# Performance work log

Hardware: AMD Instinct MI355X
Metric: run time of the kernel (lower is better)

## Reference

```python
import jax, jax.numpy as jnp
import numpy as np

D_MODEL = 1024
HEADS = 16
D_K = D_MODEL // HEADS
B, S = 2, 2048


def setup_inputs() -> dict:
    key = jax.random.key(0)
    ks = jax.random.split(key, 11)
    sc = 1.0 / np.sqrt(D_MODEL)
    return {
        "q": jax.random.normal(ks[0], (B, S, D_MODEL), jnp.float32),
        "k": jax.random.normal(ks[1], (B, S, D_MODEL), jnp.float32),
        "v": jax.random.normal(ks[2], (B, S, D_MODEL), jnp.float32),
        "Wq": jax.random.normal(ks[3], (D_MODEL, D_MODEL), jnp.float32) * sc,
        "bq": jnp.zeros((D_MODEL,), jnp.float32),
        "Wk": jax.random.normal(ks[4], (D_MODEL, D_MODEL), jnp.float32) * sc,
        "bk": jnp.zeros((D_MODEL,), jnp.float32),
        "Wv": jax.random.normal(ks[5], (D_MODEL, D_MODEL), jnp.float32) * sc,
        "bv": jnp.zeros((D_MODEL,), jnp.float32),
        "Wo": jax.random.normal(ks[6], (D_MODEL, D_MODEL), jnp.float32) * sc,
        "bo": jnp.zeros((D_MODEL,), jnp.float32),
    }


def reference(q, k, v, Wq, bq, Wk, bk, Wv, bv, Wo, bo):
    bs = q.shape[0]
    # linear projections then split heads: [B,S,D] -> [B,H,S,Dk]
    def proj(x, W, b):
        y = x @ W.T + b
        return y.reshape(bs, -1, HEADS, D_K).transpose(0, 2, 1, 3)

    qh = proj(q, Wq, bq)
    kh = proj(k, Wk, bk)
    vh = proj(v, Wv, bv)
    # scores: [B,H,Sq,Sk] -- full attention matrix as in the original
    scores = jnp.einsum("bhqd,bhkd->bhqk", qh, kh) / jnp.sqrt(
        jnp.asarray(D_K, jnp.float32))
    attn = jax.nn.softmax(scores, axis=-1)
    # dropout is identity in eval/reference mode
    out = jnp.einsum("bhqk,bhkd->bhqd", attn, vh)
    concat = out.transpose(0, 2, 1, 3).reshape(bs, -1, D_MODEL)
    return concat @ Wo.T + bo
```

## Files before the change

### kernel.cpp

```cpp
#include <hip/hip_runtime.h>
#include <hip/hip_bf16.h>

typedef __attribute__((ext_vector_type(8))) short bf16x8;
typedef __attribute__((ext_vector_type(4))) float f32x4;

#define DM   1024
#define SEQ  2048
#define NB   2
#define NH   16
#define MR   (NB*SEQ)

#define SMK  (MR*DM)
#define W1M  (DM*DM)

#define QSCALE 0.18033688011112042f

#define OFF_QB  ((size_t)0)
#define OFF_KB  ((size_t)SMK)
#define OFF_VB  ((size_t)(2*(size_t)SMK))
#define OFF_WQ  ((size_t)(3*(size_t)SMK))
#define OFF_WO  ((size_t)(3*(size_t)SMK + 3*(size_t)W1M))
#define OFF_QP  ((size_t)(3*(size_t)SMK + 4*(size_t)W1M))
#define OFF_KP  ((size_t)(4*(size_t)SMK + 4*(size_t)W1M))
#define OFF_VP  ((size_t)(5*(size_t)SMK + 4*(size_t)W1M))
#define OFF_CC  ((size_t)0)

__device__ __forceinline__ unsigned short f2bf(float f) {
  union { __hip_bfloat16 b; unsigned short u; } cv;
  cv.b = __float2bfloat16(f);
  return cv.u;
}

__global__ __launch_bounds__(256) void cvt_inputs(const float* __restrict__ q,
                                                  const float* __restrict__ k,
                                                  const float* __restrict__ v,
                                                  unsigned short* __restrict__ dst) {
  const int z = blockIdx.y;
  const float* src = (z == 0) ? q : ((z == 1) ? k : v);
  int i = blockIdx.x * 256 + threadIdx.x;
  float4 val = reinterpret_cast<const float4*>(src)[i];
  ushort4 o;
  o.x = f2bf(val.x); o.y = f2bf(val.y); o.z = f2bf(val.z); o.w = f2bf(val.w);
  reinterpret_cast<ushort4*>(dst + (size_t)z * SMK)[i] = o;
}

__global__ __launch_bounds__(256) void cvt_weights(const float* __restrict__ wq,
                                                   const float* __restrict__ wk,
                                                   const float* __restrict__ wv,
                                                   const float* __restrict__ wo,
                                                   unsigned short* __restrict__ dst) {
  const int z = blockIdx.y;
  const float* src = (z == 0) ? wq : ((z == 1) ? wk : ((z == 2) ? wv : wo));
  int i = blockIdx.x * 256 + threadIdx.x;
  float4 val = reinterpret_cast<const float4*>(src)[i];
  ushort4 o;
  o.x = f2bf(val.x); o.y = f2bf(val.y); o.z = f2bf(val.z); o.w = f2bf(val.w);
  reinterpret_cast<ushort4*>(dst + (size_t)z * W1M)[i] = o;
}

__device__ __forceinline__ void gload_lds16(const void* g, void* l) {
  __builtin_amdgcn_global_load_lds(
      (const __attribute__((address_space(1))) unsigned int*)g,
      (__attribute__((address_space(3))) unsigned int*)l,
      16, 0, 0);
}

template<int BM, int BN, bool OUT_BF16, bool BIAS_ROW>
__device__ __forceinline__ void gemm_bt_body(unsigned short* __restrict__ As,
                                             unsigned short* __restrict__ Bs,
                                             const unsigned short* __restrict__ A,
                                             const unsigned short* __restrict__ Bt,
                                             const float* __restrict__ bias,
                                             void* __restrict__ Cv,
                                             int N, int K, float scale,
                                             int brow, int bcol) {
  constexpr int MREP = BM / 32;
  constexpr int NREP = BN / 32;
  const int tid  = threadIdx.x;
  const int lane = tid & 63;
  const int w    = tid >> 6;
  const int wr   = w >> 1, wc = w & 1;

  f32x4 acc[MREP][NREP];
#pragma unroll
  for (int m = 0; m < MREP; m++)
#pragma unroll
    for (int n = 0; n < NREP; n++) acc[m][n] = (f32x4){0.f, 0.f, 0.f, 0.f};

  const int srow = lane >> 2;
  const int scol = (lane & 3) * 8;

  auto stage = [&](int buf, int k0) {
#pragma unroll
    for (int c = w; c < BM / 16; c += 4)
      gload_lds16(A + (size_t)(brow + c * 16 + srow) * K + k0 + scol,
                  (char*)As + (size_t)buf * BM * 64 + c * 1024);
#pragma unroll
    for (int c = w; c < BN / 16; c += 4)
      gload_lds16(Bt + (size_t)(bcol + c * 16 + srow) * K + k0 + scol,
                  (char*)Bs + (size_t)buf * BN * 64 + c * 1024);
  };

  stage(0, 0);
  __syncthreads();

  const int nk = K / 32;
  const int lrow_a = wr * (BM / 2) + (lane & 15);
  const int lrow_b = wc * (BN / 2) + (lane & 15);
  const int lcol   = (lane >> 4) * 8;

  for (int kt = 0; kt < nk; ++kt) {
    int buf = kt & 1;
    if (kt + 1 < nk) stage(buf ^ 1, (kt + 1) * 32);
    bf16x8 a[MREP], b[NREP];
#pragma unroll
    for (int m = 0; m < MREP; m++)
      a[m] = *(const bf16x8*)&As[(size_t)buf * BM * 32 + (lrow_a + m * 16) * 32 + lcol];
#pragma unroll
    for (int n = 0; n < NREP; n++)
      b[n] = *(const bf16x8*)&Bs[(size_t)buf * BN * 32 + (lrow_b + n * 16) * 32 + lcol];
    __builtin_amdgcn_s_setprio(1);
#pragma unroll
    for (int m = 0; m < MREP; m++)
#pragma unroll
      for (int n = 0; n < NREP; n++)
        acc[m][n] = __builtin_amdgcn_mfma_f32_16x16x32_bf16(a[m], b[n], acc[m][n], 0, 0, 0);
    __builtin_amdgcn_s_setprio(0);
    __syncthreads();
  }

  const int crow0 = brow + wr * (BM / 2);
  const int ccol0 = bcol + wc * (BN / 2);
  const int rsub  = (lane >> 4) * 4;
  const int csub  = lane & 15;
#pragma unroll
  for (int m = 0; m < MREP; m++)
#pragma unroll
    for (int n = 0; n < NREP; n++) {
      int col = ccol0 + n * 16 + csub;
      float bcol_v = BIAS_ROW ? 0.f : bias[col];
#pragma unroll
      for (int q = 0; q < 4; q++) {
        int row = crow0 + m * 16 + rsub + q;
        float bb = BIAS_ROW ? bias[row] : bcol_v;
        float v = (acc[m][n][q] + bb) * scale;
        if (OUT_BF16)
          ((unsigned short*)Cv)[(size_t)row * N + col] = f2bf(v);
        else
          ((float*)Cv)[(size_t)row * N + col] = v;
      }
    }
}

__global__ __launch_bounds__(256) void gemm_qkv(unsigned short* ws,
                                                const float* __restrict__ bq,
                                                const float* __restrict__ bk,
                                                const float* __restrict__ bv) {
  __shared__ unsigned short As[2 * 128 * 32];
  __shared__ unsigned short Bs[2 * 128 * 32];
  const int z = blockIdx.z;
  const int bid = blockIdx.x;
  if (z < 2) {
    int bx = bid & 7, by = bid >> 3;
    gemm_bt_body<128, 128, true, false>(
        As, Bs,
        ws + OFF_QB + (size_t)z * SMK, ws + OFF_WQ + (size_t)z * W1M,
        z ? bk : bq, ws + OFF_QP + (size_t)z * SMK,
        DM, DM, z ? 1.f : QSCALE, by * 128, bx * 128);
  } else {
    int bx = bid & 31, by = bid >> 5;
    gemm_bt_body<128, 128, true, true>(
        As, Bs,
        ws + OFF_WQ + 2 * W1M, ws + OFF_VB,
        bv, ws + OFF_VP,
        MR, DM, 1.f, by * 128, bx * 128);
  }
}

__global__ __launch_bounds__(256) void gemm_out(const unsigned short* __restrict__ ws,
                                                const float* __restrict__ bo,
                                                float* __restrict__ out) {
  __shared__ unsigned short As[2 * 64 * 32];
  __shared__ unsigned short Bs[2 * 128 * 32];
  gemm_bt_body<64, 128, false, false>(
      As, Bs,
      ws + OFF_CC, ws + OFF_WO, bo, out,
      DM, DM, 1.f, blockIdx.y * 64, blockIdx.x * 128);
}

__global__ __launch_bounds__(256) void flash_attn(unsigned short* ws) {
  __shared__ unsigned short Ks[2][64 * 64];
  __shared__ unsigned short Vs[2][64 * 64];
  __shared__ unsigned short Ps[4][32 * 64];

  const int tid  = threadIdx.x;
  const int lane = tid & 63;
  const int w    = tid >> 6;
  const int g    = lane >> 4;
  const int ql   = lane & 15;
  const int bid  = blockIdx.x;
  const int swzb = (bid & 7) * 64 + (bid >> 3);
  const int qblk = swzb & 15;
  const int bh   = swzb >> 4;
  const int b    = bh >> 4, h = bh & 15;

  const unsigned short* Qp = ws + OFF_QP;
  const unsigned short* Kp = ws + OFF_KP;
  const unsigned short* Vp = ws + OFF_VP;
  unsigned short* CC = ws + OFF_CC;

  const unsigned short* Kg = Kp + (size_t)(b * SEQ) * DM + h * 64;
  const unsigned short* Vg = Vp + (size_t)(h * 64) * MR + (size_t)b * SEQ;

  bf16x8 aq[2][2];
#pragma unroll
  for (int s = 0; s < 2; s++) {
    const unsigned short* qrow =
        Qp + (size_t)(b * SEQ + qblk * 128 + w * 32 + s * 16 + ql) * DM + h * 64;
    aq[s][0] = *(const bf16x8*)(qrow + g * 8);
    aq[s][1] = *(const bf16x8*)(qrow + 32 + g * 8);
  }

  const bf16x8 kOnes = {16256, 16256, 16256, 16256, 16256, 16256, 16256, 16256};

  f32x4 o_acc[2][4];
  f32x4 o_l[2];
#pragma unroll
  for (int s = 0; s < 2; s++) {
    o_l[s] = (f32x4){0.f, 0.f, 0.f, 0.f};
#pragma unroll
    for (int d = 0; d < 4; d++) o_acc[s][d] = (f32x4){0.f, 0.f, 0.f, 0.f};
  }

  auto stage = [&](unsigned short* lds, const unsigned short* gbase, int stride) {
#pragma unroll
    for (int sh = 0; sh < 2; sh++) {
      int slot = sh * 256 + w * 64 + lane;
      int srow = slot >> 3;
      int gch  = (slot & 7) ^ (srow & 7);
      gload_lds16(gbase + (size_t)srow * stride + gch * 8,
                  (char*)lds + (size_t)(sh * 256 + w * 64) * 16);
    }
  };

  stage(Ks[0], Kg, DM);
  stage(Vs[0], Vg, MR);

  unsigned short* Pw = &Ps[w][0];
  const int swq = ql & 7;

  for (int kt = 0; kt < SEQ / 64; ++kt) {
    int buf = kt & 1;
    __syncthreads();
    if (kt + 1 < SEQ / 64) {
      stage(Ks[buf ^ 1], Kg + (size_t)(kt + 1) * 64 * DM, DM);
      stage(Vs[buf ^ 1], Vg + (kt + 1) * 64, MR);
    }
    const unsigned short* Kb = Ks[buf];
    const unsigned short* Vb = Vs[buf];

    f32x4 st[2][4];
#pragma unroll
    for (int s = 0; s < 2; s++)
#pragma unroll
      for (int f = 0; f < 4; f++) st[s][f] = (f32x4){0.f, 0.f, 0.f, 0.f};
    __builtin_amdgcn_s_setprio(1);
#pragma unroll
    for (int kk = 0; kk < 2; kk++)
#pragma unroll
      for (int f = 0; f < 4; f++) {
        int sr = f * 16 + ql;
        bf16x8 ak = *(const bf16x8*)&Kb[sr * 64 + (((kk * 4 + g) ^ swq) << 3)];
        st[0][f] = __builtin_amdgcn_mfma_f32_16x16x32_bf16(ak, aq[0][kk], st[0][f], 0, 0, 0);
        st[1][f] = __builtin_amdgcn_mfma_f32_16x16x32_bf16(ak, aq[1][kk], st[1][f], 0, 0, 0);
      }
    __builtin_amdgcn_s_setprio(0);

#pragma unroll
    for (int s = 0; s < 2; s++)
#pragma unroll
      for (int f = 0; f < 4; f++) {
        ushort4 pv;
        pv.x = f2bf(__builtin_amdgcn_exp2f(st[s][f][0]));
        pv.y = f2bf(__builtin_amdgcn_exp2f(st[s][f][1]));
        pv.z = f2bf(__builtin_amdgcn_exp2f(st[s][f][2]));
        pv.w = f2bf(__builtin_amdgcn_exp2f(st[s][f][3]));
        int chunk = (f << 1) + (g >> 1);
        Pw[0] = Pw[0];
        *(ushort4*)&Pw[(s * 16 + ql) * 64 + ((chunk ^ swq) << 3) + ((g & 1) << 2)] = pv;
      }

#pragma unroll
    for (int kk = 0; kk < 2; kk++) {
      bf16x8 pb0 = *(const bf16x8*)&Pw[ql * 64 + (((kk * 4 + g) ^ swq) << 3)];
      bf16x8 pb1 = *(const bf16x8*)&Pw[(16 + ql) * 64 + (((kk * 4 + g) ^ swq) << 3)];
      __builtin_amdgcn_s_setprio(1);
      o_l[0] = __builtin_amdgcn_mfma_f32_16x16x32_bf16(kOnes, pb0, o_l[0], 0, 0, 0);
      o_l[1] = __builtin_amdgcn_mfma_f32_16x16x32_bf16(kOnes, pb1, o_l[1], 0, 0, 0);
#pragma unroll
      for (int db = 0; db < 4; db++) {
        int dr = db * 16 + ql;
        bf16x8 va = *(const bf16x8*)&Vb[dr * 64 + (((kk * 4 + g) ^ swq) << 3)];
        o_acc[0][db] = __builtin_amdgcn_mfma_f32_16x16x32_bf16(va, pb0, o_acc[0][db], 0, 0, 0);
        o_acc[1][db] = __builtin_amdgcn_mfma_f32_16x16x32_bf16(va, pb1, o_acc[1][db], 0, 0, 0);
      }
      __builtin_amdgcn_s_setprio(0);
    }
  }

#pragma unroll
  for (int s = 0; s < 2; s++) {
    float inv = 1.f / o_l[s][0];
    int qg = b * SEQ + qblk * 128 + w * 32 + s * 16 + ql;
    unsigned short* crow = CC + (size_t)qg * DM + h * 64;
#pragma unroll
    for (int db = 0; db < 4; db++) {
      ushort4 o;
      o.x = f2bf(o_acc[s][db][0] * inv);
      o.y = f2bf(o_acc[s][db][1] * inv);
      o.z = f2bf(o_acc[s][db][2] * inv);
      o.w = f2bf(o_acc[s][db][3] * inv);
      *(ushort4*)&crow[db * 16 + g * 4] = o;
    }
  }
}

extern "C" void kernel_launch(void* const* d_in, const int* in_sizes, int n_in,
                              void* d_out, int out_size, void* d_ws, size_t ws_size,
                              hipStream_t stream) {
  const float* q  = (const float*)d_in[0];
  const float* k  = (const float*)d_in[1];
  const float* v  = (const float*)d_in[2];
  const float* Wq = (const float*)d_in[3];
  const float* bq = (const float*)d_in[4];
  const float* Wk = (const float*)d_in[5];
  const float* bk = (const float*)d_in[6];
  const float* Wv = (const float*)d_in[7];
  const float* bv = (const float*)d_in[8];
  const float* Wo = (const float*)d_in[9];
  const float* bo = (const float*)d_in[10];

  unsigned short* ws = (unsigned short*)d_ws;
  float* out = (float*)d_out;

  cvt_inputs<<<dim3(SMK / 1024, 3), dim3(256), 0, stream>>>(q, k, v, ws + OFF_QB);
  cvt_weights<<<dim3(W1M / 1024, 4), dim3(256), 0, stream>>>(Wq, Wk, Wv, Wo, ws + OFF_WQ);

  gemm_qkv<<<dim3(256, 1, 3), dim3(256), 0, stream>>>(ws, bq, bk, bv);

  flash_attn<<<dim3(512), dim3(256), 0, stream>>>(ws);

  gemm_out<<<dim3(DM / 128, MR / 64, 1), dim3(256), 0, stream>>>(ws, bo, out);
}
```

Before: 128.3 us.

## Use 32x32x16 MFMA in flash attention and keep P in registers via permlane swap

The attention inner loop moves from 16x16x32 to 32x32x16 bf16 MFMA tiles, with each wave handling 32 query rows as a single tile. The probability tile is packed to bf16 with v_cvt_pk_bf16_f32 and rearranged across lane halves with v_permlane32_swap, so it is no longer written to and read back from LDS. The row sum is now accumulated with scalar adds instead of an extra MFMA against a ones vector. This is meant to remove the LDS round trip and the extra MFMAs, at the cost of more accumulator registers and exact lane-layout assumptions that must match the MFMA operand format.

New measurement: 132.7 us. 3.4% more time.

```diff
diff --git a/kernel.cpp b/kernel.cpp
--- a/kernel.cpp
+++ b/kernel.cpp
@@ -3,6 +3,7 @@
 
 typedef __attribute__((ext_vector_type(8))) short bf16x8;
 typedef __attribute__((ext_vector_type(4))) float f32x4;
+typedef __attribute__((ext_vector_type(16))) float f32x16;
 
 #define DM   1024
 #define SEQ  2048
@@ -29,6 +30,16 @@
   union { __hip_bfloat16 b; unsigned short u; } cv;
   cv.b = __float2bfloat16(f);
   return cv.u;
+}
+
+__device__ __forceinline__ unsigned int cvtpk_bf16(float lo, float hi) {
+  unsigned int r;
+  asm("v_cvt_pk_bf16_f32 %0, %1, %2" : "=v"(r) : "v"(lo), "v"(hi));
+  return r;
+}
+
+__device__ __forceinline__ void plane32_swap(unsigned int& a, unsigned int& b) {
+  asm("v_permlane32_swap_b32 %0, %1" : "+v"(a), "+v"(b));
 }
 
 __global__ __launch_bounds__(256) void cvt_inputs(const float* __restrict__ q,
@@ -191,13 +202,13 @@
 __global__ __launch_bounds__(256) void flash_attn(unsigned short* ws) {
   __shared__ unsigned short Ks[2][64 * 64];
   __shared__ unsigned short Vs[2][64 * 64];
-  __shared__ unsigned short Ps[4][32 * 64];
 
   const int tid  = threadIdx.x;
   const int lane = tid & 63;
   const int w    = tid >> 6;
-  const int g    = lane >> 4;
-  const int ql   = lane & 15;
+  const int q    = lane & 31;
+  const int hi   = lane >> 5;
+  const int swq  = q & 7;
   const int bid  = blockIdx.x;
   const int swzb = (bid & 7) * 64 + (bid >> 3);
   const int qblk = swzb & 15;
@@ -212,25 +223,21 @@
   const unsigned short* Kg = Kp + (size_t)(b * SEQ) * DM + h * 64;
   const unsigned short* Vg = Vp + (size_t)(h * 64) * MR + (size_t)b * SEQ;
 
-  bf16x8 aq[2][2];
-#pragma unroll
-  for (int s = 0; s < 2; s++) {
+  bf16x8 bqf[4];
+  {
     const unsigned short* qrow =
-        Qp + (size_t)(b * SEQ + qblk * 128 + w * 32 + s * 16 + ql) * DM + h * 64;
-    aq[s][0] = *(const bf16x8*)(qrow + g * 8);
-    aq[s][1] = *(const bf16x8*)(qrow + 32 + g * 8);
+        Qp + (size_t)(b * SEQ + qblk * 128 + w * 32 + q) * DM + h * 64;
+#pragma unroll
+    for (int c = 0; c < 4; c++)
+      bqf[c] = *(const bf16x8*)(qrow + c * 16 + hi * 8);
   }
 
-  const bf16x8 kOnes = {16256, 16256, 16256, 16256, 16256, 16256, 16256, 16256};
-
-  f32x4 o_acc[2][4];
-  f32x4 o_l[2];
-#pragma unroll
-  for (int s = 0; s < 2; s++) {
-    o_l[s] = (f32x4){0.f, 0.f, 0.f, 0.f};
-#pragma unroll
-    for (int d = 0; d < 4; d++) o_acc[s][d] = (f32x4){0.f, 0.f, 0.f, 0.f};
-  }
+  f32x16 o_acc[2];
+#pragma unroll
+  for (int dt = 0; dt < 2; dt++)
+#pragma unroll
+    for (int r = 0; r < 16; r++) o_acc[dt][r] = 0.f;
+  float l_run = 0.f;
 
   auto stage = [&](unsigned short* lds, const unsigned short* gbase, int stride) {
 #pragma unroll
@@ -246,9 +253,6 @@
   stage(Ks[0], Kg, DM);
   stage(Vs[0], Vg, MR);
 
-  unsigned short* Pw = &Ps[w][0];
-  const int swq = ql & 7;
-
   for (int kt = 0; kt < SEQ / 64; ++kt) {
     int buf = kt & 1;
     __syncthreads();
@@ -259,70 +263,73 @@
     const unsigned short* Kb = Ks[buf];
     const unsigned short* Vb = Vs[buf];
 
-    f32x4 st[2][4];
-#pragma unroll
-    for (int s = 0; s < 2; s++)
-#pragma unroll
-      for (int f = 0; f < 4; f++) st[s][f] = (f32x4){0.f, 0.f, 0.f, 0.f};
+    f32x16 st0, st1;
+#pragma unroll
+    for (int r = 0; r < 16; r++) { st0[r] = 0.f; st1[r] = 0.f; }
     __builtin_amdgcn_s_setprio(1);
 #pragma unroll
-    for (int kk = 0; kk < 2; kk++)
-#pragma unroll
-      for (int f = 0; f < 4; f++) {
-        int sr = f * 16 + ql;
-        bf16x8 ak = *(const bf16x8*)&Kb[sr * 64 + (((kk * 4 + g) ^ swq) << 3)];
-        st[0][f] = __builtin_amdgcn_mfma_f32_16x16x32_bf16(ak, aq[0][kk], st[0][f], 0, 0, 0);
-        st[1][f] = __builtin_amdgcn_mfma_f32_16x16x32_bf16(ak, aq[1][kk], st[1][f], 0, 0, 0);
+    for (int c = 0; c < 4; c++) {
+      int ch = (((c << 1) | hi) ^ swq) << 3;
+      bf16x8 ak0 = *(const bf16x8*)&Kb[q * 64 + ch];
+      bf16x8 ak1 = *(const bf16x8*)&Kb[(32 + q) * 64 + ch];
+      st0 = __builtin_amdgcn_mfma_f32_32x32x16_bf16(ak0, bqf[c], st0, 0, 0, 0);
+      st1 = __builtin_amdgcn_mfma_f32_32x32x16_bf16(ak1, bqf[c], st1, 0, 0, 0);
+    }
+    __builtin_amdgcn_s_setprio(0);
+
+    unsigned int pk0[8], pk1[8];
+    float lt = 0.f;
+#pragma unroll
+    for (int p = 0; p < 8; p++) {
+      float a0 = __builtin_amdgcn_exp2f(st0[2 * p]);
+      float a1 = __builtin_amdgcn_exp2f(st0[2 * p + 1]);
+      float b0 = __builtin_amdgcn_exp2f(st1[2 * p]);
+      float b1 = __builtin_amdgcn_exp2f(st1[2 * p + 1]);
+      lt += (a0 + a1) + (b0 + b1);
+      pk0[p] = cvtpk_bf16(a0, a1);
+      pk1[p] = cvtpk_bf16(b0, b1);
+    }
+    l_run += lt;
+
+    plane32_swap(pk0[0], pk0[2]); plane32_swap(pk0[1], pk0[3]);
+    plane32_swap(pk0[4], pk0[6]); plane32_swap(pk0[5], pk0[7]);
+    plane32_swap(pk1[0], pk1[2]); plane32_swap(pk1[1], pk1[3]);
+    plane32_swap(pk1[4], pk1[6]); plane32_swap(pk1[5], pk1[7]);
+
+    __builtin_amdgcn_s_setprio(1);
+#pragma unroll
+    for (int t = 0; t < 4; t++) {
+      union { unsigned int u[4]; bf16x8 v; } pb;
+      const unsigned int* src = (t < 2) ? pk0 : pk1;
+      pb.u[0] = src[(t & 1) * 4 + 0];
+      pb.u[1] = src[(t & 1) * 4 + 1];
+      pb.u[2] = src[(t & 1) * 4 + 2];
+      pb.u[3] = src[(t & 1) * 4 + 3];
+      int ch = (((t << 1) | hi) ^ swq) << 3;
+#pragma unroll
+      for (int dt = 0; dt < 2; dt++) {
+        bf16x8 av = *(const bf16x8*)&Vb[(dt * 32 + q) * 64 + ch];
+        o_acc[dt] = __builtin_amdgcn_mfma_f32_32x32x16_bf16(av, pb.v, o_acc[dt], 0, 0, 0);
       }
+    }
     __builtin_amdgcn_s_setprio(0);
-
-#pragma unroll
-    for (int s = 0; s < 2; s++)
-#pragma unroll
-      for (int f = 0; f < 4; f++) {
-        ushort4 pv;
-        pv.x = f2bf(__builtin_amdgcn_exp2f(st[s][f][0]));
-        pv.y = f2bf(__builtin_amdgcn_exp2f(st[s][f][1]));
-        pv.z = f2bf(__builtin_amdgcn_exp2f(st[s][f][2]));
-        pv.w = f2bf(__builtin_amdgcn_exp2f(st[s][f][3]));
-        int chunk = (f << 1) + (g >> 1);
-        Pw[0] = Pw[0];
-        *(ushort4*)&Pw[(s * 16 + ql) * 64 + ((chunk ^ swq) << 3) + ((g & 1) << 2)] = pv;
-      }
-
-#pragma unroll
-    for (int kk = 0; kk < 2; kk++) {
-      bf16x8 pb0 = *(const bf16x8*)&Pw[ql * 64 + (((kk * 4 + g) ^ swq) << 3)];
-      bf16x8 pb1 = *(const bf16x8*)&Pw[(16 + ql) * 64 + (((kk * 4 + g) ^ swq) << 3)];
-      __builtin_amdgcn_s_setprio(1);
-      o_l[0] = __builtin_amdgcn_mfma_f32_16x16x32_bf16(kOnes, pb0, o_l[0], 0, 0, 0);
-      o_l[1] = __builtin_amdgcn_mfma_f32_16x16x32_bf16(kOnes, pb1, o_l[1], 0, 0, 0);
-#pragma unroll
-      for (int db = 0; db < 4; db++) {
-        int dr = db * 16 + ql;
-        bf16x8 va = *(const bf16x8*)&Vb[dr * 64 + (((kk * 4 + g) ^ swq) << 3)];
-        o_acc[0][db] = __builtin_amdgcn_mfma_f32_16x16x32_bf16(va, pb0, o_acc[0][db], 0, 0, 0);
-        o_acc[1][db] = __builtin_amdgcn_mfma_f32_16x16x32_bf16(va, pb1, o_acc[1][db], 0, 0, 0);
-      }
-      __builtin_amdgcn_s_setprio(0);
-    }
   }
 
-#pragma unroll
-  for (int s = 0; s < 2; s++) {
-    float inv = 1.f / o_l[s][0];
-    int qg = b * SEQ + qblk * 128 + w * 32 + s * 16 + ql;
-    unsigned short* crow = CC + (size_t)qg * DM + h * 64;
-#pragma unroll
-    for (int db = 0; db < 4; db++) {
+  float l = l_run + __shfl_xor(l_run, 32, 64);
+  float inv = 1.f / l;
+  int qg = b * SEQ + qblk * 128 + w * 32 + q;
+  unsigned short* crow = CC + (size_t)qg * DM + h * 64;
+#pragma unroll
+  for (int dt = 0; dt < 2; dt++)
+#pragma unroll
+    for (int rq = 0; rq < 4; rq++) {
       ushort4 o;
-      o.x = f2bf(o_acc[s][db][0] * inv);
-      o.y = f2bf(o_acc[s][db][1] * inv);
-      o.z = f2bf(o_acc[s][db][2] * inv);
-      o.w = f2bf(o_acc[s][db][3] * inv);
-      *(ushort4*)&crow[db * 16 + g * 4] = o;
-    }
-  }
+      o.x = f2bf(o_acc[dt][4 * rq + 0] * inv);
+      o.y = f2bf(o_acc[dt][4 * rq + 1] * inv);
+      o.z = f2bf(o_acc[dt][4 * rq + 2] * inv);
+      o.w = f2bf(o_acc[dt][4 * rq + 3] * inv);
+      *(ushort4*)&crow[dt * 32 + rq * 8 + hi * 4] = o;
+    }
 }
 
 extern "C" void kernel_launch(void* const* d_in, const int* in_sizes, int n_in,
```
